# Kernel tuning notes

Measured on AMD Instinct MI355X. Metric: run time of the kernel, lower is better.

The kernel has to match this reference:

```python
import jax, jax.numpy as jnp
import numpy as np

B, P, K_NN, HEADS = 4, 2048, 30, 3
N = B * P


def knn_nbr(feat):
    """Per-cloud exact KNN (no self), returns [N, K_NN+1] global neighbor idx, self appended last.
    Matches torch_geometric knn_graph (loop=False) followed by GATConv add_self_loops=True."""
    f = feat.reshape(B, P, -1)
    sq = jnp.sum(f * f, axis=-1)  # [B,P]
    d = sq[:, :, None] + sq[:, None, :] - 2.0 * jnp.einsum('bpc,bqc->bpq', f, f)
    d = d + jnp.eye(P, dtype=f.dtype)[None] * 1e9  # exclude self
    idx = jax.lax.top_k(-d, K_NN)[1]  # [B,P,K_NN] nearest neighbors
    idx = (idx + (jnp.arange(B) * P)[:, None, None]).reshape(N, K_NN)
    return jnp.concatenate([idx, jnp.arange(N)[:, None]], axis=1)  # self-loop last


def gat(xf, nbr, W, a_src, a_dst, bias):
    """PyG GATConv (v1, concat=True, negative_slope=0.2). nbr: [N,K] incoming sources per node."""
    H, F = a_src.shape
    xh = (xf @ W).reshape(N, H, F)
    s = jnp.sum(xh * a_src, axis=-1)  # [N,H] source scores
    t = jnp.sum(xh * a_dst, axis=-1)  # [N,H] target scores
    e = jax.nn.leaky_relu(s[nbr] + t[:, None, :], 0.2)  # [N,K,H]
    alpha = jax.nn.softmax(e, axis=1)  # edge-softmax over incoming edges
    out = jnp.einsum('nkh,nkhf->nhf', alpha, xh[nbr])
    return out.reshape(N, H * F) + bias


def setup_inputs() -> dict:
    key = jax.random.key(0)
    ks = jax.random.split(key, 48)
    w = lambda k, shape: (jax.random.normal(k, shape, jnp.float32) * 0.1)
    H = HEADS
    inp = {
        'x': jax.random.normal(ks[0], (N, 3), jnp.float32),
        'pos': jax.random.normal(ks[1], (N, 3), jnp.float32),
        'batch': (jnp.arange(N) // P).astype(jnp.int32),
        'w1': w(ks[2], (6, 64 * H)), 'as1': w(ks[3], (H, 64)), 'ad1': w(ks[4], (H, 64)), 'b1': w(ks[5], (64 * H,)),
        'ml1w': w(ks[6], (64 * H, 64)), 'ml1b': w(ks[7], (64,)),
        'w2': w(ks[8], (70, 64 * H)), 'as2': w(ks[9], (H, 64)), 'ad2': w(ks[10], (H, 64)), 'b2': w(ks[11], (64 * H,)),
        'ml2w': w(ks[12], (64 * H, 64)), 'ml2b': w(ks[13], (64,)),
        'w3': w(ks[14], (134, 64 * H)), 'as3': w(ks[15], (H, 64)), 'ad3': w(ks[16], (H, 64)), 'b3': w(ks[17], (64 * H,)),
        'ml3w': w(ks[18], (64 * H, 64)), 'ml3b': w(ks[19], (64,)),
        'w4': w(ks[20], (198, 128 * H)), 'as4': w(ks[21], (H, 128)), 'ad4': w(ks[22], (H, 128)), 'b4': w(ks[23], (128 * H,)),
        'ml4w': w(ks[24], (128 * H, 128)), 'ml4b': w(ks[25], (128,)),
        # fe_mlp: 326 -> 1024 -> 1024 (plain last)
        'few1': w(ks[26], (326, 1024)), 'feb1': w(ks[27], (1024,)),
        'few2': w(ks[28], (1024, 1024)), 'feb2': w(ks[29], (1024,)),
        # head mlp: 1350 -> 256 -> 256 -> 128 -> 50
        'mw1': w(ks[30], (1350, 256)), 'mb1': w(ks[31], (256,)),
        'mw2': w(ks[32], (256, 256)), 'mb2': w(ks[33], (256,)),
        'mw3': w(ks[34], (256, 128)), 'mb3': w(ks[35], (128,)),
        'mw4': w(ks[36], (128, 50)), 'mb4': w(ks[37], (50,)),
    }
    return inp


def reference(x, pos, batch,
              w1, as1, ad1, b1, ml1w, ml1b,
              w2, as2, ad2, b2, ml2w, ml2b,
              w3, as3, ad3, b3, ml3w, ml3b,
              w4, as4, ad4, b4, ml4w, ml4b,
              few1, feb1, few2, feb2,
              mw1, mb1, mw2, mb2, mw3, mb3, mw4, mb4):
    x0 = jnp.concatenate([x, pos], axis=-1)  # [N,6]
    nbr = knn_nbr(x0)
    x1 = gat(x0, nbr, w1, as1, ad1, b1) @ ml1w + ml1b  # [N,64]
    nbr = knn_nbr(x1)
    x2 = gat(jnp.concatenate([x0, x1], 1), nbr, w2, as2, ad2, b2) @ ml2w + ml2b
    nbr = knn_nbr(x2)
    x3 = gat(jnp.concatenate([x0, x1, x2], 1), nbr, w3, as3, ad3, b3) @ ml3w + ml3b
    nbr = knn_nbr(x2)  # faithful to source: 4th graph also built from x2
    x4 = gat(jnp.concatenate([x0, x1, x2, x3], 1), nbr, w4, as4, ad4, b4) @ ml4w + ml4b
    link4 = jnp.concatenate([x0, x1, x2, x3, x4], axis=-1)  # [N,326]
    h = jax.nn.relu(link4 @ few1 + feb1) @ few2 + feb2  # [N,1024]
    g = jnp.max(h, axis=0, keepdims=True)  # global feature (dropout=eval identity)
    lg = jnp.concatenate([link4, jnp.broadcast_to(g, (N, h.shape[1]))], axis=1)
    h = jax.nn.relu(lg @ mw1 + mb1)
    h = jax.nn.relu(h @ mw2 + mb2)
    h = jax.nn.relu(h @ mw3 + mb3)
    out = h @ mw4 + mb4
    return jax.nn.log_softmax(out, axis=1)
```

## Files before the change

### kernel.cpp

```cpp
#include <hip/hip_runtime.h>
#include <hip/hip_bf16.h>
#include <hip/amd_detail/amd_hip_vector_types.h>

#define NPTS 8192
#define PP 2048
#define KNN 30
#define KTOT 31
#define HEADS 3
#define LDH 352
#define NSEG 10

typedef __attribute__((ext_vector_type(8))) short short8;
typedef __attribute__((ext_vector_type(4))) float floatx4;
typedef __attribute__((ext_vector_type(4))) unsigned int uint4_t;
typedef unsigned short ushort_t;
typedef unsigned int uint_t;

__device__ inline ushort_t f2bs(float v) {
    __hip_bfloat16 b = __float2bfloat16(v);
    return *reinterpret_cast<ushort_t*>(&b);
}
__device__ inline float bs2f(ushort_t u) {
    __hip_bfloat16 b = *reinterpret_cast<__hip_bfloat16*>(&u);
    return __bfloat162float(b);
}
__device__ inline void split2(float v, ushort_t& h, ushort_t& l) {
    h = f2bs(v);
    l = f2bs(v - bs2f(h));
}
__device__ inline uint_t fenc(float f) {
    uint_t b = __float_as_uint(f);
    return (b & 0x80000000u) ? ~b : (b | 0x80000000u);
}
__device__ inline float fdec(uint_t e) {
    return __uint_as_float((e & 0x80000000u) ? (e & 0x7FFFFFFFu) : ~e);
}

__global__ void k_build_x0(const float* __restrict__ x, const float* __restrict__ pos,
                           ushort_t* __restrict__ lh, ushort_t* __restrict__ ll) {
    int i = blockIdx.x * blockDim.x + threadIdx.x;
    if (i >= NPTS * 6) return;
    int n = i / 6, c = i % 6;
    float v = (c < 3) ? x[n * 3 + c] : pos[n * 3 + (c - 3)];
    ushort_t h, l; split2(v, h, l);
    lh[(size_t)n * LDH + c] = h;
    ll[(size_t)n * LDH + c] = l;
}

__global__ void k_tw1(const float* __restrict__ x, const float* __restrict__ pos,
                      const float* __restrict__ w1, float* __restrict__ xh) {
    int t = blockIdx.x * blockDim.x + threadIdx.x;
    if (t >= NPTS * 192) return;
    int n = t / 192, j = t % 192;
    float acc = 0.f;
#pragma unroll
    for (int c = 0; c < 3; c++) {
        acc += x[n * 3 + c] * w1[c * 192 + j];
        acc += pos[n * 3 + c] * w1[(3 + c) * 192 + j];
    }
    xh[(size_t)n * 192 + j] = acc;
}

struct WArgs {
    const float* src[NSEG];
    ushort_t* dst[NSEG];
    int K[NSEG], N[NSEG], Kp[NSEG], t0[NSEG];
};
__global__ void k_wsplit_all(WArgs a) {
    int bt = blockIdx.x;
    int si = 0;
#pragma unroll
    for (int i = 1; i < NSEG; i++) if (bt >= a.t0[i]) si = i;
    int t = bt - a.t0[si];
    int K_ = a.K[si], N_ = a.N[si], Kp = a.Kp[si];
    const float* src = a.src[si];
    ushort_t* dh = a.dst[si];
    ushort_t* dl = dh + (size_t)Kp * N_;
    int tX = (N_ + 31) >> 5;
    int k0 = (t / tX) * 32, n0 = (t % tX) * 32;
    __shared__ float tt[32][33];
    int c = threadIdx.x & 31, r8 = threadIdx.x >> 5;
#pragma unroll
    for (int i = 0; i < 4; i++) {
        int r = r8 + i * 8;
        int k = k0 + r, n = n0 + c;
        tt[r][c] = (k < K_ && n < N_) ? src[(size_t)k * N_ + n] : 0.f;
    }
    __syncthreads();
#pragma unroll
    for (int i = 0; i < 4; i++) {
        int r = r8 + i * 8;
        int n = n0 + r, k = k0 + c;
        if (n < N_) {
            float v = tt[c][r];
            ushort_t h, l; split2(v, h, l);
            dh[(size_t)n * Kp + k] = h;
            dl[(size_t)n * Kp + k] = l;
        }
    }
}

template<int MT, int NT>
__global__ __launch_bounds__(256)
void k_mgemm1(const ushort_t* __restrict__ A, int lda,
              const ushort_t* __restrict__ W, int ldw,
              float* __restrict__ Cf, int ldc,
              ushort_t* __restrict__ Ch, int ldh,
              int Ndim, int K,
              const float* __restrict__ bias1, const float* __restrict__ bias2,
              int relu, int lsm, uint_t* __restrict__ gmax,
              const float* __restrict__ asrc, const float* __restrict__ adst,
              float* __restrict__ sb, float* __restrict__ tb, int Fsc, int satomic) {
    constexpr int MTW = MT / 64;
    constexpr int NTT = NT / 16;
    __shared__ ushort_t As[2][MT * 40];
    __shared__ ushort_t Bs[2][NT * 40];
    __shared__ uint_t smax[NT];
    int tid = threadIdx.x;
    int w = tid >> 6, lane = tid & 63;
    int quad = lane >> 4, l16 = lane & 15;
    int m0 = blockIdx.x * MT, n0 = blockIdx.y * NT;
    uint4_t pa[MT / 64], pb[NT / 64];
    auto prefetch = [&](int k0) {
#pragma unroll
        for (int rep = 0; rep < MT / 64; rep++) {
            int idx = tid + rep * 256;
            int row = idx >> 2, q = idx & 3;
            pa[rep] = *(const uint4_t*)(A + (size_t)(m0 + row) * lda + k0 + q * 8);
        }
#pragma unroll
        for (int rep = 0; rep < NT / 64; rep++) {
            int idx = tid + rep * 256;
            int row = idx >> 2, q = idx & 3;
            uint4_t v = {0, 0, 0, 0};
            if (n0 + row < Ndim) v = *(const uint4_t*)(W + (size_t)(n0 + row) * ldw + k0 + q * 8);
            pb[rep] = v;
        }
    };
    auto stage = [&](int buf) {
#pragma unroll
        for (int rep = 0; rep < MT / 64; rep++) {
            int idx = tid + rep * 256;
            int row = idx >> 2, q = idx & 3;
            *(uint4_t*)&As[buf][row * 40 + q * 8] = pa[rep];
        }
#pragma unroll
        for (int rep = 0; rep < NT / 64; rep++) {
            int idx = tid + rep * 256;
            int row = idx >> 2, q = idx & 3;
            *(uint4_t*)&Bs[buf][row * 40 + q * 8] = pb[rep];
        }
    };
    if (gmax) {
        for (int idx = tid; idx < NT; idx += 256) smax[idx] = 0u;
    }
    floatx4 acc[MTW][NTT] = {};
    prefetch(0);
    stage(0);
    __syncthreads();
    int cur = 0;
    for (int k0 = 0; k0 < K; k0 += 32) {
        bool more = (k0 + 32 < K);
        if (more) prefetch(k0 + 32);
        short8 ah[MTW];
#pragma unroll
        for (int mt = 0; mt < MTW; mt++) {
            int r = w * (MT / 4) + mt * 16 + l16;
            ah[mt] = *(short8*)&As[cur][r * 40 + quad * 8];
        }
#pragma unroll
        for (int nt = 0; nt < NTT; nt++) {
            int r = nt * 16 + l16;
            short8 bh = *(short8*)&Bs[cur][r * 40 + quad * 8];
#pragma unroll
            for (int mt = 0; mt < MTW; mt++)
                acc[mt][nt] = __builtin_amdgcn_mfma_f32_16x16x32_bf16(ah[mt], bh, acc[mt][nt], 0, 0, 0);
        }
        if (more) stage(cur ^ 1);
        __syncthreads();
        cur ^= 1;
    }
    if (lsm) {
#pragma unroll
        for (int mt = 0; mt < MTW; mt++) {
#pragma unroll
            for (int r = 0; r < 4; r++) {
                float vv[NTT];
                float mrow = -3e38f;
#pragma unroll
                for (int nt = 0; nt < NTT; nt++) {
                    int n = n0 + nt * 16 + l16;
                    float val = (n < Ndim) ? acc[mt][nt][r] + bias1[n] : -3e38f;
                    vv[nt] = val;
                    mrow = fmaxf(mrow, val);
                }
#pragma unroll
                for (int off = 8; off >= 1; off >>= 1)
                    mrow = fmaxf(mrow, __shfl_xor(mrow, off, 64));
                float s = 0.f;
#pragma unroll
                for (int nt = 0; nt < NTT; nt++)
                    if (vv[nt] > -1e38f) s += expf(vv[nt] - mrow);
#pragma unroll
                for (int off = 8; off >= 1; off >>= 1)
                    s += __shfl_xor(s, off, 64);
                float lse = mrow + logf(s);
                int m = m0 + w * (MT / 4) + mt * 16 + quad * 4 + r;
#pragma unroll
                for (int nt = 0; nt < NTT; nt++) {
                    int n = n0 + nt * 16 + l16;
                    if (n < Ndim) Cf[(size_t)m * ldc + n] = vv[nt] - lse;
                }
            }
        }
        return;
    }
    if (gmax) {
#pragma unroll
        for (int mt = 0; mt < MTW; mt++) {
#pragma unroll
            for (int nt = 0; nt < NTT; nt++) {
#pragma unroll
                for (int r = 0; r < 4; r++) {
                    float v = acc[mt][nt][r] + bias1[nt * 16 + l16 + n0];
                    atomicMax(&smax[nt * 16 + l16], fenc(v));
                }
            }
        }
        __syncthreads();
        for (int idx = tid; idx < NT; idx += 256)
            atomicMax(&gmax[n0 + idx], smax[idx]);
        return;
    }
    if (asrc) {
        int h = n0 / Fsc;
#pragma unroll
        for (int mt = 0; mt < MTW; mt++) {
#pragma unroll
            for (int r = 0; r < 4; r++) {
                float sp = 0.f, tp = 0.f;
#pragma unroll
                for (int nt = 0; nt < NTT; nt++) {
                    float v = acc[mt][nt][r];
                    sp += v * asrc[n0 + nt * 16 + l16];
                    tp += v * adst[n0 + nt * 16 + l16];
                }
#pragma unroll
                for (int off = 8; off >= 1; off >>= 1) {
                    sp += __shfl_xor(sp, off, 64);
                    tp += __shfl_xor(tp, off, 64);
                }
                if (l16 == 0) {
                    int m = m0 + w * (MT / 4) + mt * 16 + quad * 4 + r;
                    if (satomic) {
                        atomicAdd(&sb[m * HEADS + h], sp);
                        atomicAdd(&tb[m * HEADS + h], tp);
                    } else {
                        sb[m * HEADS + h] = sp;
                        tb[m * HEADS + h] = tp;
                    }
                }
            }
        }
    }
#pragma unroll
    for (int mt = 0; mt < MTW; mt++) {
#pragma unroll
        for (int nt = 0; nt < NTT; nt++) {
#pragma unroll
            for (int r = 0; r < 4; r++) {
                int m = m0 + w * (MT / 4) + mt * 16 + quad * 4 + r;
                int n = n0 + nt * 16 + l16;
                if (n < Ndim) {
                    float v = acc[mt][nt][r];
                    if (bias1) v += bias1[n];
                    if (bias2) v += bias2[n];
                    if (relu && v < 0.f) v = 0.f;
                    if (Cf) Cf[(size_t)m * ldc + n] = v;
                    if (Ch) Ch[(size_t)m * ldh + n] = f2bs(v);
                }
            }
        }
    }
}

__global__ __launch_bounds__(256)
void k_mgemm3(const ushort_t* __restrict__ Ah, const ushort_t* __restrict__ Al, int lda,
              const ushort_t* __restrict__ Wh, const ushort_t* __restrict__ Wl, int ldw,
              float* __restrict__ Cf, int ldc,
              int Ndim, int K,
              const float* __restrict__ asrc, const float* __restrict__ adst,
              float* __restrict__ sb, float* __restrict__ tb, int Fsc) {
    constexpr int NTT = 4;
    __shared__ ushort_t AsH[64 * 40], BsH[64 * 40], AsL[64 * 40], BsL[64 * 40];
    int tid = threadIdx.x;
    int w = tid >> 6, lane = tid & 63;
    int quad = lane >> 4, l16 = lane & 15;
    int m0 = blockIdx.y * 64, n0 = blockIdx.x * 64;
    floatx4 acc[NTT] = {};
    for (int k0 = 0; k0 < K; k0 += 32) {
        {
            int row = tid >> 2, q = tid & 3;
            size_t go = (size_t)(m0 + row) * lda + k0 + q * 8;
            *(uint4_t*)&AsH[row * 40 + q * 8] = *(const uint4_t*)(Ah + go);
            *(uint4_t*)&AsL[row * 40 + q * 8] = *(const uint4_t*)(Al + go);
            uint4_t vh = {0, 0, 0, 0}, vl = {0, 0, 0, 0};
            size_t gw = (size_t)(n0 + row) * ldw + k0 + q * 8;
            if (n0 + row < Ndim) { vh = *(const uint4_t*)(Wh + gw); vl = *(const uint4_t*)(Wl + gw); }
            *(uint4_t*)&BsH[row * 40 + q * 8] = vh;
            *(uint4_t*)&BsL[row * 40 + q * 8] = vl;
        }
        __syncthreads();
        short8 ah, al;
        {
            int r = w * 16 + l16;
            ah = *(short8*)&AsH[r * 40 + quad * 8];
            al = *(short8*)&AsL[r * 40 + quad * 8];
        }
#pragma unroll
        for (int nt = 0; nt < NTT; nt++) {
            int r = nt * 16 + l16;
            short8 bh = *(short8*)&BsH[r * 40 + quad * 8];
            short8 bl = *(short8*)&BsL[r * 40 + quad * 8];
            acc[nt] = __builtin_amdgcn_mfma_f32_16x16x32_bf16(ah, bh, acc[nt], 0, 0, 0);
            acc[nt] = __builtin_amdgcn_mfma_f32_16x16x32_bf16(ah, bl, acc[nt], 0, 0, 0);
            acc[nt] = __builtin_amdgcn_mfma_f32_16x16x32_bf16(al, bh, acc[nt], 0, 0, 0);
        }
        __syncthreads();
    }
    if (asrc) {
        int h = n0 / Fsc;
#pragma unroll
        for (int r = 0; r < 4; r++) {
            float sp = 0.f, tp = 0.f;
#pragma unroll
            for (int nt = 0; nt < NTT; nt++) {
                float v = acc[nt][r];
                sp += v * asrc[n0 + nt * 16 + l16];
                tp += v * adst[n0 + nt * 16 + l16];
            }
#pragma unroll
            for (int off = 8; off >= 1; off >>= 1) {
                sp += __shfl_xor(sp, off, 64);
                tp += __shfl_xor(tp, off, 64);
            }
            if (l16 == 0) {
                int m = m0 + w * 16 + quad * 4 + r;
                sb[m * HEADS + h] = sp;
                tb[m * HEADS + h] = tp;
            }
        }
    }
#pragma unroll
    for (int nt = 0; nt < NTT; nt++) {
#pragma unroll
        for (int r = 0; r < 4; r++) {
            int m = m0 + w * 16 + quad * 4 + r;
            int n = n0 + nt * 16 + l16;
            if (n < Ndim) Cf[(size_t)m * ldc + n] = acc[nt][r];
        }
    }
}

template<int N_, int NPB>
__global__ __launch_bounds__(NPB * N_)
void k_vgemm(const float* __restrict__ A, int lda, int K_,
             const float* __restrict__ W, const float* __restrict__ bias,
             ushort_t* __restrict__ Ch, ushort_t* __restrict__ Cl, int ldh,
             float* __restrict__ Cf, int ldc, int relu) {
    constexpr int KT = 64;
    __shared__ float Ws[KT * N_];
    __shared__ float As[NPB * KT];
    int t = threadIdx.x;
    int n0 = blockIdx.x * NPB;
    int node = t / N_, j = t % N_;
    float acc = bias ? bias[j] : 0.f;
    for (int k0 = 0; k0 < K_; k0 += KT) {
        for (int idx = t; idx < KT * N_; idx += NPB * N_)
            Ws[idx] = W[(size_t)(k0 + idx / N_) * N_ + idx % N_];
        for (int idx = t; idx < NPB * KT; idx += NPB * N_)
            As[idx] = A[(size_t)(n0 + idx / KT) * lda + k0 + idx % KT];
        __syncthreads();
#pragma unroll
        for (int kk = 0; kk < KT; kk++)
            acc += As[node * KT + kk] * Ws[kk * N_ + j];
        __syncthreads();
    }
    if (relu && acc < 0.f) acc = 0.f;
    size_t m = n0 + node;
    if (Cf) Cf[m * ldc + j] = acc;
    if (Ch) {
        ushort_t h = f2bs(acc);
        Ch[m * ldh + j] = h;
        if (Cl) Cl[m * ldh + j] = f2bs(acc - bs2f(h));
    }
}

__global__ __launch_bounds__(256)
void k_mdist(const ushort_t* __restrict__ Lh, const ushort_t* __restrict__ Ll,
             int co, int C, uint_t* __restrict__ keys) {
    __shared__ ushort_t AsH[128 * 40], AsL[128 * 40], BsH[64 * 40], BsL[64 * 40];
    __shared__ float sqa[128], sqb[64];
    int tid = threadIdx.x;
    int w = tid >> 6, lane = tid & 63;
    int quad = lane >> 4, l16 = lane & 15;
    int b = blockIdx.z, cb = b * PP;
    int i0 = blockIdx.y * 128, j0 = blockIdx.x * 64;
    floatx4 acc[2][4] = {};
    float sacc = 0.f;
    for (int k0 = 0; k0 < C; k0 += 32) {
#pragma unroll
        for (int rep = 0; rep < 8; rep++) {
            int d = tid + rep * 256;
            int row = d >> 4, c2 = d & 15;
            size_t gi = ((size_t)(cb + i0 + row) * LDH + co + k0 + c2 * 2) >> 1;
            *(uint_t*)&AsH[row * 40 + c2 * 2] = ((const uint_t*)Lh)[gi];
            *(uint_t*)&AsL[row * 40 + c2 * 2] = ((const uint_t*)Ll)[gi];
        }
#pragma unroll
        for (int rep = 0; rep < 4; rep++) {
            int d = tid + rep * 256;
            int row = d >> 4, c2 = d & 15;
            size_t gi = ((size_t)(cb + j0 + row) * LDH + co + k0 + c2 * 2) >> 1;
            *(uint_t*)&BsH[row * 40 + c2 * 2] = ((const uint_t*)Lh)[gi];
            *(uint_t*)&BsL[row * 40 + c2 * 2] = ((const uint_t*)Ll)[gi];
        }
        __syncthreads();
        if (tid < 128) {
#pragma unroll
            for (int kk = 0; kk < 16; kk++) {
                uint_t ph = *(uint_t*)&AsH[tid * 40 + kk * 2];
                uint_t pl = *(uint_t*)&AsL[tid * 40 + kk * 2];
                float v0 = bs2f((ushort_t)(ph & 0xFFFFu)) + bs2f((ushort_t)(pl & 0xFFFFu));
                sacc += v0 * v0;
                float v1 = bs2f((ushort_t)(ph >> 16)) + bs2f((ushort_t)(pl >> 16));
                sacc += v1 * v1;
            }
        } else if (tid < 192) {
            int row = tid - 128;
#pragma unroll
            for (int kk = 0; kk < 16; kk++) {
                uint_t ph = *(uint_t*)&BsH[row * 40 + kk * 2];
                uint_t pl = *(uint_t*)&BsL[row * 40 + kk * 2];
                float v0 = bs2f((ushort_t)(ph & 0xFFFFu)) + bs2f((ushort_t)(pl & 0xFFFFu));
                sacc += v0 * v0;
                float v1 = bs2f((ushort_t)(ph >> 16)) + bs2f((ushort_t)(pl >> 16));
                sacc += v1 * v1;
            }
        }
        short8 ah[2], al[2];
#pragma unroll
        for (int mt = 0; mt < 2; mt++) {
            int r = w * 32 + mt * 16 + l16;
            ah[mt] = *(short8*)&AsH[r * 40 + quad * 8];
            al[mt] = *(short8*)&AsL[r * 40 + quad * 8];
        }
#pragma unroll
        for (int nt = 0; nt < 4; nt++) {
            int r = nt * 16 + l16;
            short8 bh = *(short8*)&BsH[r * 40 + quad * 8];
            short8 bl = *(short8*)&BsL[r * 40 + quad * 8];
#pragma unroll
            for (int mt = 0; mt < 2; mt++) {
                acc[mt][nt] = __builtin_amdgcn_mfma_f32_16x16x32_bf16(ah[mt], bh, acc[mt][nt], 0, 0, 0);
                acc[mt][nt] = __builtin_amdgcn_mfma_f32_16x16x32_bf16(ah[mt], bl, acc[mt][nt], 0, 0, 0);
                acc[mt][nt] = __builtin_amdgcn_mfma_f32_16x16x32_bf16(al[mt], bh, acc[mt][nt], 0, 0, 0);
            }
        }
        __syncthreads();
    }
    if (tid < 128) sqa[tid] = sacc;
    else if (tid < 192) sqb[tid - 128] = sacc;
    __syncthreads();
#pragma unroll
    for (int mt = 0; mt < 2; mt++) {
#pragma unroll
        for (int nt = 0; nt < 4; nt++) {
#pragma unroll
            for (int r = 0; r < 4; r++) {
                int li = w * 32 + mt * 16 + quad * 4 + r;
                int lj = nt * 16 + l16;
                int il = i0 + li, jl = j0 + lj;
                float dd = sqa[li] + sqb[lj] - 2.f * acc[mt][nt][r];
                dd = (il == jl) ? 3e9f : fmaxf(dd, 0.f);
                uint_t key = (__float_as_uint(dd) & 0xFFFFF800u) | (uint_t)jl;
                __builtin_nontemporal_store(key, &keys[(size_t)(cb + il) * PP + jl]);
            }
        }
    }
}

__global__ __launch_bounds__(256)
void k_topk(const uint_t* __restrict__ keys, int* __restrict__ nbr) {
    int r = blockIdx.x * 4 + (threadIdx.x >> 6);
    int lane = threadIdx.x & 63;
    int base = (r / PP) * PP;
    const uint_t* row = keys + (size_t)r * PP;
    uint_t v[32];
#pragma unroll
    for (int j = 0; j < 8; j++)
        *(uint4_t*)&v[j * 4] = *(const uint4_t*)(row + lane * 4 + j * 256);
    uint_t g[8];
#pragma unroll
    for (int j = 0; j < 8; j++)
        g[j] = min(min(v[j * 4], v[j * 4 + 1]), min(v[j * 4 + 2], v[j * 4 + 3]));
    uint_t lv = g[0];
#pragma unroll
    for (int j = 1; j < 8; j++) lv = min(lv, g[j]);
    for (int sel = 0; sel < KNN; sel++) {
        uint_t bk = lv;
#pragma unroll
        for (int off = 32; off > 0; off >>= 1)
            bk = min(bk, (uint_t)__shfl_xor((int)bk, off, 64));
        uint_t bks = __builtin_amdgcn_readfirstlane(bk);
        if (lane == 0) nbr[r * KTOT + sel] = base + (int)(bks & 0x7FFu);
        int grp = (int)((bks & 0x7FFu) >> 8);
#pragma unroll
        for (int jj = 0; jj < 8; jj++)
            if (grp == jj) {
#pragma unroll
                for (int t = 0; t < 4; t++)
                    v[jj * 4 + t] = (v[jj * 4 + t] == bks) ? 0xFFFFFFFFu : v[jj * 4 + t];
                g[jj] = min(min(v[jj * 4], v[jj * 4 + 1]), min(v[jj * 4 + 2], v[jj * 4 + 3]));
            }
        lv = g[0];
#pragma unroll
        for (int j = 1; j < 8; j++) lv = min(lv, g[j]);
    }
    if (lane == 0) nbr[r * KTOT + KNN] = r;
}

__global__ void k_scores(const float* __restrict__ xh, int F,
                         const float* __restrict__ a_src,
                         const float* __restrict__ a_dst,
                         float* __restrict__ s, float* __restrict__ t) {
    int g = blockIdx.x * blockDim.x + threadIdx.x;
    if (g >= NPTS * HEADS) return;
    int n = g / HEADS, h = g % HEADS;
    const float* xr = xh + (size_t)n * (HEADS * F) + h * F;
    float ss = 0.f, tt = 0.f;
    for (int f = 0; f < F; f++) {
        float v = xr[f];
        ss += v * a_src[h * F + f];
        tt += v * a_dst[h * F + f];
    }
    s[g] = ss;
    t[g] = tt;
}

__global__ void k_gat(const float* __restrict__ xh, int F,
                      const float* __restrict__ s, const float* __restrict__ t,
                      const int* __restrict__ nbr,
                      const float* __restrict__ bias,
                      float* __restrict__ outf, ushort_t* __restrict__ oh) {
    int HF = HEADS * F;
    __shared__ int srcs[KTOT];
    __shared__ float alpha[KTOT * HEADS];
    int i = (blockIdx.x & 3) * PP + (blockIdx.x >> 2);
    int tid = threadIdx.x;
    if (tid < KTOT) srcs[tid] = nbr[i * KTOT + tid];
    __syncthreads();
    if (tid < KTOT * HEADS) {
        int k = tid / HEADS, h = tid % HEADS;
        float e = s[srcs[k] * HEADS + h] + t[i * HEADS + h];
        if (e < 0.f) e *= 0.2f;
        alpha[tid] = e;
    }
    __syncthreads();
    if (tid < HEADS) {
        int h = tid;
        float m = -3e38f;
        for (int k = 0; k < KTOT; k++) m = fmaxf(m, alpha[k * HEADS + h]);
        float sum = 0.f;
        for (int k = 0; k < KTOT; k++) {
            float ex = expf(alpha[k * HEADS + h] - m);
            alpha[k * HEADS + h] = ex;
            sum += ex;
        }
        float inv = 1.f / sum;
        for (int k = 0; k < KTOT; k++) alpha[k * HEADS + h] *= inv;
    }
    __syncthreads();
    int h = tid / F;
    float acc = 0.f;
    for (int k = 0; k < KTOT; k++)
        acc += alpha[k * HEADS + h] * xh[(size_t)srcs[k] * HF + tid];
    float v = acc + bias[tid];
    if (oh) oh[(size_t)i * HF + tid] = f2bs(v);
    else outf[(size_t)i * HF + tid] = v;
}

__global__ void k_gproj(const uint_t* __restrict__ genc,
                        const float* __restrict__ mw1,
                        const float* __restrict__ mb1,
                        float* __restrict__ gproj) {
    __shared__ float gs[128];
    int kb = blockIdx.x;
    int t = threadIdx.x;
    if (t < 128) gs[t] = fdec(genc[kb * 128 + t]);
    __syncthreads();
    float acc = (kb == 0) ? mb1[t] : 0.f;
    for (int k = 0; k < 128; k++)
        acc += gs[k] * mw1[(size_t)(326 + kb * 128 + k) * 256 + t];
    atomicAdd(&gproj[t], acc);
}

struct WT { ushort_t *h, *l; int kp; };

extern "C" void kernel_launch(void* const* d_in, const int* in_sizes, int n_in,
                              void* d_out, int out_size, void* d_ws, size_t ws_size,
                              hipStream_t stream) {
    (void)in_sizes; (void)n_in; (void)out_size; (void)ws_size;
    const float* x    = (const float*)d_in[0];
    const float* pos  = (const float*)d_in[1];
    const float* w1   = (const float*)d_in[3];
    const float* as1  = (const float*)d_in[4];
    const float* ad1  = (const float*)d_in[5];
    const float* b1   = (const float*)d_in[6];
    const float* ml1w = (const float*)d_in[7];
    const float* ml1b = (const float*)d_in[8];
    const float* w2   = (const float*)d_in[9];
    const float* as2  = (const float*)d_in[10];
    const float* ad2  = (const float*)d_in[11];
    const float* b2   = (const float*)d_in[12];
    const float* ml2w = (const float*)d_in[13];
    const float* ml2b = (const float*)d_in[14];
    const float* w3   = (const float*)d_in[15];
    const float* as3  = (const float*)d_in[16];
    const float* ad3  = (const float*)d_in[17];
    const float* b3   = (const float*)d_in[18];
    const float* ml3w = (const float*)d_in[19];
    const float* ml3b = (const float*)d_in[20];
    const float* w4   = (const float*)d_in[21];
    const float* as4  = (const float*)d_in[22];
    const float* ad4  = (const float*)d_in[23];
    const float* b4   = (const float*)d_in[24];
    const float* ml4w = (const float*)d_in[25];
    const float* ml4b = (const float*)d_in[26];
    const float* few1 = (const float*)d_in[27];
    const float* feb1 = (const float*)d_in[28];
    const float* few2 = (const float*)d_in[29];
    const float* feb2 = (const float*)d_in[30];
    const float* mw1  = (const float*)d_in[31];
    const float* mb1  = (const float*)d_in[32];
    const float* mw2  = (const float*)d_in[33];
    const float* mb2  = (const float*)d_in[34];
    const float* mw3  = (const float*)d_in[35];
    const float* mb3  = (const float*)d_in[36];
    const float* mw4  = (const float*)d_in[37];
    const float* mb4  = (const float*)d_in[38];

    float* Wb = (float*)d_ws;
    size_t off = 0;
    auto alloc = [&](size_t n) { float* p = Wb + off; off += (n + 63) & ~(size_t)63; return p; };

    float*    dist = alloc((size_t)NPTS * PP);
    ushort_t* l4h  = (ushort_t*)alloc((size_t)NPTS * LDH / 2);
    ushort_t* l4l  = (ushort_t*)alloc((size_t)NPTS * LDH / 2);
    float*    gof  = alloc((size_t)NPTS * 384);
    ushort_t* goh  = (ushort_t*)alloc((size_t)NPTS * 384 / 2);
    float* sbuf  = alloc((size_t)NPTS * HEADS);
    float* tbuf  = alloc((size_t)NPTS * HEADS);
    float* s4   = alloc((size_t)NPTS * HEADS);
    float* t4   = alloc((size_t)NPTS * HEADS);
    uint_t* genc = (uint_t*)alloc(1024);
    float* gproj = alloc(256);
    int*   nbr   = (int*)alloc((size_t)NPTS * KTOT);
    ushort_t* wtpool = (ushort_t*)alloc(1831168 + 128);

    char* d0 = (char*)dist;
    uint_t*   dkey = (uint_t*)dist;
    float*    xh   = dist;
    ushort_t* hah  = (ushort_t*)d0;
    ushort_t* bBh  = (ushort_t*)(d0 + (size_t)NPTS * 1024 * 2);
    ushort_t* bAh = (ushort_t*)gof;
    ushort_t* bCh = (ushort_t*)gof;

    hipMemsetAsync(l4h, 0, (size_t)NPTS * LDH * 4, stream);
    hipMemsetAsync(gproj, 0, 256 * 4, stream);
    hipMemsetAsync(genc, 0, 1024 * 4, stream);
    hipMemsetAsync(s4, 0, (size_t)NPTS * HEADS * 2 * 4, stream);

    WArgs wa;
    WT wt[NSEG];
    {
        const float* srcs[NSEG] = {w2, w3, w4, ml4w, few1, few2, mw1, mw2, mw3, mw4};
        int Ks[NSEG] = {70, 134, 198, 384, 326, 1024, 326, 256, 256, 128};
        int Ns[NSEG] = {192, 192, 384, 128, 1024, 1024, 256, 256, 128, 50};
        size_t wo = 0; int tiles = 0;
        for (int i = 0; i < NSEG; i++) {
            int kp = (Ks[i] + 31) & ~31;
            wa.src[i] = srcs[i];
            wa.dst[i] = wtpool + wo;
            wa.K[i] = Ks[i]; wa.N[i] = Ns[i]; wa.Kp[i] = kp;
            wa.t0[i] = tiles;
            wt[i] = { wtpool + wo, wtpool + wo + (size_t)kp * Ns[i], kp };
            wo += (size_t)2 * kp * Ns[i];
            tiles += (kp / 32) * ((Ns[i] + 31) / 32);
        }
        k_wsplit_all<<<tiles, 256, 0, stream>>>(wa);
    }
    WT tw2 = wt[0], tw3 = wt[1], tw4 = wt[2], tml4 = wt[3], tfe1 = wt[4], tfe2 = wt[5],
       tmw1 = wt[6], tmw2 = wt[7], tmw3 = wt[8], tmw4 = wt[9];

    auto mg3 = [&](const ushort_t* Ah, const ushort_t* Al, int lda, WT t,
                   float* Cf, int ldc, int Nd, int K,
                   const float* asrc, const float* adst, float* sb, float* tb, int Fsc) {
        dim3 g((Nd + 63) / 64, NPTS / 64);
        k_mgemm3<<<g, 256, 0, stream>>>(Ah, Al, lda, t.h, t.l, t.kp, Cf, ldc, Nd, K,
                                        asrc, adst, sb, tb, Fsc);
    };
    auto mg1 = [&](int MT, int NT, const ushort_t* Ah, int lda, WT t,
                   float* Cf, int ldc, ushort_t* Ch, int ldhh,
                   int Nd, int K, const float* bb1, const float* bb2,
                   int relu, int lsm, uint_t* gmax,
                   const float* asrc, const float* adst, float* sb, float* tb,
                   int Fsc, int satomic) {
        dim3 g(NPTS / MT, (Nd + NT - 1) / NT);
        if (MT == 128 && NT == 64)
            k_mgemm1<128, 64><<<g, 256, 0, stream>>>(Ah, lda, t.h, t.kp, Cf, ldc, Ch, ldhh, Nd, K,
                bb1, bb2, relu, lsm, gmax, asrc, adst, sb, tb, Fsc, satomic);
        else
            k_mgemm1<64, 64><<<g, 256, 0, stream>>>(Ah, lda, t.h, t.kp, Cf, ldc, Ch, ldhh, Nd, K,
                bb1, bb2, relu, lsm, gmax, asrc, adst, sb, tb, Fsc, satomic);
    };

    dim3 dgrid(PP / 64, PP / 128, 4);
    k_build_x0<<<(NPTS * 6 + 255) / 256, 256, 0, stream>>>(x, pos, l4h, l4l);

    k_mdist<<<dgrid, 256, 0, stream>>>(l4h, l4l, 0, 6, dkey);
    k_topk<<<NPTS / 4, 256, 0, stream>>>(dkey, nbr);
    k_tw1<<<(NPTS * 192 + 255) / 256, 256, 0, stream>>>(x, pos, w1, xh);
    k_scores<<<(NPTS * HEADS + 255) / 256, 256, 0, stream>>>(xh, 64, as1, ad1, sbuf, tbuf);
    k_gat<<<NPTS, 192, 0, stream>>>(xh, 64, sbuf, tbuf, nbr, b1, gof, nullptr);
    k_vgemm<64, 4><<<NPTS / 4, 256, 0, stream>>>(gof, 192, 192, ml1w, ml1b,
        l4h + 6, l4l + 6, LDH, nullptr, 0, 0);

    k_mdist<<<dgrid, 256, 0, stream>>>(l4h, l4l, 6, 64, dkey);
    k_topk<<<NPTS / 4, 256, 0, stream>>>(dkey, nbr);
    mg3(l4h, l4l, LDH, tw2, xh, 192, 192, 70, as2, ad2, sbuf, tbuf, 64);
    k_gat<<<NPTS, 192, 0, stream>>>(xh, 64, sbuf, tbuf, nbr, b2, gof, nullptr);
    k_vgemm<64, 4><<<NPTS / 4, 256, 0, stream>>>(gof, 192, 192, ml2w, ml2b,
        l4h + 70, l4l + 70, LDH, nullptr, 0, 0);

    k_mdist<<<dgrid, 256, 0, stream>>>(l4h, l4l, 70, 64, dkey);
    k_topk<<<NPTS / 4, 256, 0, stream>>>(dkey, nbr);
    mg1(64, 64, l4h, LDH, tw3, xh, 192, nullptr, 0, 192, 134, nullptr, nullptr, 0, 0, nullptr,
        as3, ad3, sbuf, tbuf, 64, 0);
    k_gat<<<NPTS, 192, 0, stream>>>(xh, 64, sbuf, tbuf, nbr, b3, gof, nullptr);
    k_vgemm<64, 4><<<NPTS / 4, 256, 0, stream>>>(gof, 192, 192, ml3w, ml3b,
        l4h + 134, nullptr, LDH, nullptr, 0, 0);

    mg1(64, 64, l4h, LDH, tw4, xh, 384, nullptr, 0, 384, 198, nullptr, nullptr, 0, 0, nullptr,
        as4, ad4, s4, t4, 128, 1);
    k_gat<<<NPTS, 384, 0, stream>>>(xh, 128, s4, t4, nbr, b4, nullptr, goh);
    mg1(64, 64, goh, 384, tml4, nullptr, 0, l4h + 198, LDH, 128, 384, ml4b, nullptr, 0, 0, nullptr,
        nullptr, nullptr, nullptr, nullptr, 1, 0);

    mg1(128, 64, l4h, LDH, tfe1, nullptr, 0, hah, 1024, 1024, 326, feb1, nullptr, 1, 0, nullptr,
        nullptr, nullptr, nullptr, nullptr, 1, 0);
    mg1(128, 64, hah, 1024, tfe2, nullptr, 0, nullptr, 0, 1024, 1024, feb2, nullptr, 0, 0, genc,
        nullptr, nullptr, nullptr, nullptr, 1, 0);
    k_gproj<<<8, 256, 0, stream>>>(genc, mw1, mb1, gproj);

    mg1(128, 64, l4h, LDH, tmw1, nullptr, 0, bAh, 256, 256, 326, nullptr, gproj, 1, 0, nullptr,
        nullptr, nullptr, nullptr, nullptr, 1, 0);
    mg1(128, 64, bAh, 256, tmw2, nullptr, 0, bBh, 256, 256, 256, mb2, nullptr, 1, 0, nullptr,
        nullptr, nullptr, nullptr, nullptr, 1, 0);
    mg1(64, 64, bBh, 256, tmw3, nullptr, 0, bCh, 128, 128, 256, mb3, nullptr, 1, 0, nullptr,
        nullptr, nullptr, nullptr, nullptr, 1, 0);
    mg1(64, 64, bCh, 128, tmw4, (float*)d_out, 50, nullptr, 0, 50, 128, mb4, nullptr, 0, 1, nullptr,
        nullptr, nullptr, nullptr, nullptr, 1, 0);
}
```

Baseline: 615.3 us.

## Fold GAT output projection and attention vectors into combined weights

Precomputes combined weights W·mlW per head, plus W·a_src and W·a_dst columns and a folded bias, in a new k_combine kernel. Each GAT layer's per-node GEMM then directly produces projected per-head features and attention scores. The aggregation kernel sums the per-head contributions and writes bf16 hi/lo into the feature buffer, which removes the separate score kernel, the post-GAT linear GEMMs and the intermediate buffers. It also switches the fe1/fe2 GEMMs to 128x128 tiles. The risk is changed rounding from reassociating the linear maps, which could slightly alter the KNN neighbour selection in later layers.

```diff
diff --git a/kernel.cpp b/kernel.cpp
--- a/kernel.cpp
+++ b/kernel.cpp
@@ -8,7 +8,9 @@
 #define KTOT 31
 #define HEADS 3
 #define LDH 352
-#define NSEG 10
+#define NSEG 9
+#define LDZ 200
+#define LDZ4 392
 
 typedef __attribute__((ext_vector_type(8))) short short8;
 typedef __attribute__((ext_vector_type(4))) float floatx4;
@@ -47,18 +49,61 @@
     ll[(size_t)n * LDH + c] = l;
 }
 
+struct CArgs {
+    const float *w[4], *mlw[4], *as_[4], *ad[4], *b[4], *mlb[4];
+    float *wc[4], *bc[4];
+    int K[4], F[4], t0[4];
+};
+__global__ void k_combine(CArgs a) {
+    int bt = blockIdx.x, si = 0;
+#pragma unroll
+    for (int i = 1; i < 4; i++) if (bt >= a.t0[i]) si = i;
+    int t = (bt - a.t0[si]) * 256 + threadIdx.x;
+    int K_ = a.K[si], F_ = a.F[si];
+    int NC = 3 * F_ + 6;
+    const float* w = a.w[si];
+    const float* mlw = a.mlw[si];
+    if (t < K_ * NC) {
+        int k = t / NC, c = t % NC;
+        float acc = 0.f;
+        if (c < 3 * F_) {
+            int h = c / F_, j = c % F_;
+            for (int f = 0; f < F_; f++)
+                acc += w[(size_t)k * 3 * F_ + h * F_ + f] * mlw[(size_t)(h * F_ + f) * F_ + j];
+        } else if (c < 3 * F_ + 3) {
+            int h = c - 3 * F_;
+            const float* av = a.as_[si];
+            for (int f = 0; f < F_; f++)
+                acc += w[(size_t)k * 3 * F_ + h * F_ + f] * av[h * F_ + f];
+        } else {
+            int h = c - 3 * F_ - 3;
+            const float* av = a.ad[si];
+            for (int f = 0; f < F_; f++)
+                acc += w[(size_t)k * 3 * F_ + h * F_ + f] * av[h * F_ + f];
+        }
+        a.wc[si][t] = acc;
+    } else if (t < K_ * NC + F_) {
+        int j = t - K_ * NC;
+        float acc = a.mlb[si][j];
+        const float* b = a.b[si];
+        for (int c = 0; c < 3 * F_; c++)
+            acc += b[c] * mlw[(size_t)c * F_ + j];
+        a.bc[si][j] = acc;
+    }
+}
+
 __global__ void k_tw1(const float* __restrict__ x, const float* __restrict__ pos,
-                      const float* __restrict__ w1, float* __restrict__ xh) {
+                      const float* __restrict__ wc, float* __restrict__ z) {
     int t = blockIdx.x * blockDim.x + threadIdx.x;
-    if (t >= NPTS * 192) return;
-    int n = t / 192, j = t % 192;
+    if (t >= NPTS * 198) return;
+    int n = t / 198, j = t % 198;
     float acc = 0.f;
 #pragma unroll
     for (int c = 0; c < 3; c++) {
-        acc += x[n * 3 + c] * w1[c * 192 + j];
-        acc += pos[n * 3 + c] * w1[(3 + c) * 192 + j];
-    }
-    xh[(size_t)n * 192 + j] = acc;
+        acc += x[n * 3 + c] * wc[c * 198 + j];
+        acc += pos[n * 3 + c] * wc[(3 + c) * 198 + j];
+    }
+    z[(size_t)n * LDZ + j] = acc;
 }
 
 struct WArgs {
@@ -108,9 +153,7 @@
               ushort_t* __restrict__ Ch, int ldh,
               int Ndim, int K,
               const float* __restrict__ bias1, const float* __restrict__ bias2,
-              int relu, int lsm, uint_t* __restrict__ gmax,
-              const float* __restrict__ asrc, const float* __restrict__ adst,
-              float* __restrict__ sb, float* __restrict__ tb, int Fsc, int satomic) {
+              int relu, int lsm, uint_t* __restrict__ gmax) {
     constexpr int MTW = MT / 64;
     constexpr int NTT = NT / 16;
     __shared__ ushort_t As[2][MT * 40];
@@ -231,37 +274,6 @@
         for (int idx = tid; idx < NT; idx += 256)
             atomicMax(&gmax[n0 + idx], smax[idx]);
         return;
-    }
-    if (asrc) {
-        int h = n0 / Fsc;
-#pragma unroll
-        for (int mt = 0; mt < MTW; mt++) {
-#pragma unroll
-            for (int r = 0; r < 4; r++) {
-                float sp = 0.f, tp = 0.f;
-#pragma unroll
-                for (int nt = 0; nt < NTT; nt++) {
-                    float v = acc[mt][nt][r];
-                    sp += v * asrc[n0 + nt * 16 + l16];
-                    tp += v * adst[n0 + nt * 16 + l16];
-                }
-#pragma unroll
-                for (int off = 8; off >= 1; off >>= 1) {
-                    sp += __shfl_xor(sp, off, 64);
-                    tp += __shfl_xor(tp, off, 64);
-                }
-                if (l16 == 0) {
-                    int m = m0 + w * (MT / 4) + mt * 16 + quad * 4 + r;
-                    if (satomic) {
-                        atomicAdd(&sb[m * HEADS + h], sp);
-                        atomicAdd(&tb[m * HEADS + h], tp);
-                    } else {
-                        sb[m * HEADS + h] = sp;
-                        tb[m * HEADS + h] = tp;
-                    }
-                }
-            }
-        }
     }
 #pragma unroll
     for (int mt = 0; mt < MTW; mt++) {
@@ -288,9 +300,7 @@
 void k_mgemm3(const ushort_t* __restrict__ Ah, const ushort_t* __restrict__ Al, int lda,
               const ushort_t* __restrict__ Wh, const ushort_t* __restrict__ Wl, int ldw,
               float* __restrict__ Cf, int ldc,
-              int Ndim, int K,
-              const float* __restrict__ asrc, const float* __restrict__ adst,
-              float* __restrict__ sb, float* __restrict__ tb, int Fsc) {
+              int Ndim, int K) {
     constexpr int NTT = 4;
     __shared__ ushort_t AsH[64 * 40], BsH[64 * 40], AsL[64 * 40], BsL[64 * 40];
     int tid = threadIdx.x;
@@ -328,29 +338,6 @@
         }
         __syncthreads();
     }
-    if (asrc) {
-        int h = n0 / Fsc;
-#pragma unroll
-        for (int r = 0; r < 4; r++) {
-            float sp = 0.f, tp = 0.f;
-#pragma unroll
-            for (int nt = 0; nt < NTT; nt++) {
-                float v = acc[nt][r];
-                sp += v * asrc[n0 + nt * 16 + l16];
-                tp += v * adst[n0 + nt * 16 + l16];
-            }
-#pragma unroll
-            for (int off = 8; off >= 1; off >>= 1) {
-                sp += __shfl_xor(sp, off, 64);
-                tp += __shfl_xor(tp, off, 64);
-            }
-            if (l16 == 0) {
-                int m = m0 + w * 16 + quad * 4 + r;
-                sb[m * HEADS + h] = sp;
-                tb[m * HEADS + h] = tp;
-            }
-        }
-    }
 #pragma unroll
     for (int nt = 0; nt < NTT; nt++) {
 #pragma unroll
@@ -359,40 +346,6 @@
             int n = n0 + nt * 16 + l16;
             if (n < Ndim) Cf[(size_t)m * ldc + n] = acc[nt][r];
         }
-    }
-}
-
-template<int N_, int NPB>
-__global__ __launch_bounds__(NPB * N_)
-void k_vgemm(const float* __restrict__ A, int lda, int K_,
-             const float* __restrict__ W, const float* __restrict__ bias,
-             ushort_t* __restrict__ Ch, ushort_t* __restrict__ Cl, int ldh,
-             float* __restrict__ Cf, int ldc, int relu) {
-    constexpr int KT = 64;
-    __shared__ float Ws[KT * N_];
-    __shared__ float As[NPB * KT];
-    int t = threadIdx.x;
-    int n0 = blockIdx.x * NPB;
-    int node = t / N_, j = t % N_;
-    float acc = bias ? bias[j] : 0.f;
-    for (int k0 = 0; k0 < K_; k0 += KT) {
-        for (int idx = t; idx < KT * N_; idx += NPB * N_)
-            Ws[idx] = W[(size_t)(k0 + idx / N_) * N_ + idx % N_];
-        for (int idx = t; idx < NPB * KT; idx += NPB * N_)
-            As[idx] = A[(size_t)(n0 + idx / KT) * lda + k0 + idx % KT];
-        __syncthreads();
-#pragma unroll
-        for (int kk = 0; kk < KT; kk++)
-            acc += As[node * KT + kk] * Ws[kk * N_ + j];
-        __syncthreads();
-    }
-    if (relu && acc < 0.f) acc = 0.f;
-    size_t m = n0 + node;
-    if (Cf) Cf[m * ldc + j] = acc;
-    if (Ch) {
-        ushort_t h = f2bs(acc);
-        Ch[m * ldh + j] = h;
-        if (Cl) Cl[m * ldh + j] = f2bs(acc - bs2f(h));
     }
 }
 
@@ -530,39 +483,22 @@
     if (lane == 0) nbr[r * KTOT + KNN] = r;
 }
 
-__global__ void k_scores(const float* __restrict__ xh, int F,
-                         const float* __restrict__ a_src,
-                         const float* __restrict__ a_dst,
-                         float* __restrict__ s, float* __restrict__ t) {
-    int g = blockIdx.x * blockDim.x + threadIdx.x;
-    if (g >= NPTS * HEADS) return;
-    int n = g / HEADS, h = g % HEADS;
-    const float* xr = xh + (size_t)n * (HEADS * F) + h * F;
-    float ss = 0.f, tt = 0.f;
-    for (int f = 0; f < F; f++) {
-        float v = xr[f];
-        ss += v * a_src[h * F + f];
-        tt += v * a_dst[h * F + f];
-    }
-    s[g] = ss;
-    t[g] = tt;
-}
-
-__global__ void k_gat(const float* __restrict__ xh, int F,
-                      const float* __restrict__ s, const float* __restrict__ t,
-                      const int* __restrict__ nbr,
-                      const float* __restrict__ bias,
-                      float* __restrict__ outf, ushort_t* __restrict__ oh) {
-    int HF = HEADS * F;
+template<int F>
+__global__ __launch_bounds__(3 * F)
+void k_gat2(const float* __restrict__ z, int ldz,
+            const int* __restrict__ nbr,
+            const float* __restrict__ bc,
+            ushort_t* __restrict__ dh, ushort_t* __restrict__ dl) {
     __shared__ int srcs[KTOT];
     __shared__ float alpha[KTOT * HEADS];
+    __shared__ float part[HEADS * F];
     int i = (blockIdx.x & 3) * PP + (blockIdx.x >> 2);
     int tid = threadIdx.x;
     if (tid < KTOT) srcs[tid] = nbr[i * KTOT + tid];
     __syncthreads();
     if (tid < KTOT * HEADS) {
         int k = tid / HEADS, h = tid % HEADS;
-        float e = s[srcs[k] * HEADS + h] + t[i * HEADS + h];
+        float e = z[(size_t)srcs[k] * ldz + 3 * F + h] + z[(size_t)i * ldz + 3 * F + 3 + h];
         if (e < 0.f) e *= 0.2f;
         alpha[tid] = e;
     }
@@ -581,13 +517,18 @@
         for (int k = 0; k < KTOT; k++) alpha[k * HEADS + h] *= inv;
     }
     __syncthreads();
-    int h = tid / F;
+    int h = tid / F, j = tid % F;
     float acc = 0.f;
     for (int k = 0; k < KTOT; k++)
-        acc += alpha[k * HEADS + h] * xh[(size_t)srcs[k] * HF + tid];
-    float v = acc + bias[tid];
-    if (oh) oh[(size_t)i * HF + tid] = f2bs(v);
-    else outf[(size_t)i * HF + tid] = v;
+        acc += alpha[k * HEADS + h] * z[(size_t)srcs[k] * ldz + h * F + j];
+    part[h * F + j] = acc;
+    __syncthreads();
+    if (tid < F) {
+        float v = part[tid] + part[F + tid] + part[2 * F + tid] + bc[tid];
+        ushort_t hi = f2bs(v);
+        dh[(size_t)i * LDH + tid] = hi;
+        if (dl) dl[(size_t)i * LDH + tid] = f2bs(v - bs2f(hi));
+    }
 }
 
 __global__ void k_gproj(const uint_t* __restrict__ genc,
@@ -657,36 +598,58 @@
     float*    dist = alloc((size_t)NPTS * PP);
     ushort_t* l4h  = (ushort_t*)alloc((size_t)NPTS * LDH / 2);
     ushort_t* l4l  = (ushort_t*)alloc((size_t)NPTS * LDH / 2);
-    float*    gof  = alloc((size_t)NPTS * 384);
-    ushort_t* goh  = (ushort_t*)alloc((size_t)NPTS * 384 / 2);
-    float* sbuf  = alloc((size_t)NPTS * HEADS);
-    float* tbuf  = alloc((size_t)NPTS * HEADS);
-    float* s4   = alloc((size_t)NPTS * HEADS);
-    float* t4   = alloc((size_t)NPTS * HEADS);
     uint_t* genc = (uint_t*)alloc(1024);
     float* gproj = alloc(256);
     int*   nbr   = (int*)alloc((size_t)NPTS * KTOT);
-    ushort_t* wtpool = (ushort_t*)alloc(1831168 + 128);
+    ushort_t* wtpool = (ushort_t*)alloc(1742336);
+    float* wc1 = alloc(6 * 198);
+    float* wc2 = alloc(70 * 198);
+    float* wc3 = alloc(134 * 198);
+    float* wc4 = alloc(198 * 390);
+    float* bc1 = alloc(64);
+    float* bc2 = alloc(64);
+    float* bc3 = alloc(64);
+    float* bc4 = alloc(128);
 
     char* d0 = (char*)dist;
     uint_t*   dkey = (uint_t*)dist;
-    float*    xh   = dist;
+    float*    z    = dist;
     ushort_t* hah  = (ushort_t*)d0;
     ushort_t* bBh  = (ushort_t*)(d0 + (size_t)NPTS * 1024 * 2);
-    ushort_t* bAh = (ushort_t*)gof;
-    ushort_t* bCh = (ushort_t*)gof;
+    ushort_t* bAh = (ushort_t*)d0;
+    ushort_t* bCh = (ushort_t*)d0;
 
     hipMemsetAsync(l4h, 0, (size_t)NPTS * LDH * 4, stream);
     hipMemsetAsync(gproj, 0, 256 * 4, stream);
     hipMemsetAsync(genc, 0, 1024 * 4, stream);
-    hipMemsetAsync(s4, 0, (size_t)NPTS * HEADS * 2 * 4, stream);
+
+    {
+        CArgs ca;
+        const float* ws_[4] = {w1, w2, w3, w4};
+        const float* mlws[4] = {ml1w, ml2w, ml3w, ml4w};
+        const float* ass[4] = {as1, as2, as3, as4};
+        const float* ads[4] = {ad1, ad2, ad3, ad4};
+        const float* bs_[4] = {b1, b2, b3, b4};
+        const float* mlbs[4] = {ml1b, ml2b, ml3b, ml4b};
+        float* wcs[4] = {wc1, wc2, wc3, wc4};
+        float* bcs[4] = {bc1, bc2, bc3, bc4};
+        int Ks[4] = {6, 70, 134, 198}, Fs[4] = {64, 64, 64, 128};
+        int t = 0;
+        for (int i = 0; i < 4; i++) {
+            ca.w[i] = ws_[i]; ca.mlw[i] = mlws[i]; ca.as_[i] = ass[i]; ca.ad[i] = ads[i];
+            ca.b[i] = bs_[i]; ca.mlb[i] = mlbs[i]; ca.wc[i] = wcs[i]; ca.bc[i] = bcs[i];
+            ca.K[i] = Ks[i]; ca.F[i] = Fs[i]; ca.t0[i] = t;
+            t += (Ks[i] * (3 * Fs[i] + 6) + Fs[i] + 255) / 256;
+        }
+        k_combine<<<t, 256, 0, stream>>>(ca);
+    }
 
     WArgs wa;
     WT wt[NSEG];
     {
-        const float* srcs[NSEG] = {w2, w3, w4, ml4w, few1, few2, mw1, mw2, mw3, mw4};
-        int Ks[NSEG] = {70, 134, 198, 384, 326, 1024, 326, 256, 256, 128};
-        int Ns[NSEG] = {192, 192, 384, 128, 1024, 1024, 256, 256, 128, 50};
+        const float* srcs[NSEG] = {wc2, wc3, wc4, few1, few2, mw1, mw2, mw3, mw4};
+        int Ks[NSEG] = {70, 134, 198, 326, 1024, 326, 256, 256, 128};
+        int Ns[NSEG] = {198, 198, 390, 1024, 1024, 256, 256, 128, 50};
         size_t wo = 0; int tiles = 0;
         for (int i = 0; i < NSEG; i++) {
             int kp = (Ks[i] + 31) & ~31;
@@ -700,29 +663,28 @@
         }
         k_wsplit_all<<<tiles, 256, 0, stream>>>(wa);
     }
-    WT tw2 = wt[0], tw3 = wt[1], tw4 = wt[2], tml4 = wt[3], tfe1 = wt[4], tfe2 = wt[5],
-       tmw1 = wt[6], tmw2 = wt[7], tmw3 = wt[8], tmw4 = wt[9];
+    WT tw2 = wt[0], tw3 = wt[1], tw4 = wt[2], tfe1 = wt[3], tfe2 = wt[4],
+       tmw1 = wt[5], tmw2 = wt[6], tmw3 = wt[7], tmw4 = wt[8];
 
     auto mg3 = [&](const ushort_t* Ah, const ushort_t* Al, int lda, WT t,
-                   float* Cf, int ldc, int Nd, int K,
-                   const float* asrc, const float* adst, float* sb, float* tb, int Fsc) {
+                   float* Cf, int ldc, int Nd, int K) {
         dim3 g((Nd + 63) / 64, NPTS / 64);
-        k_mgemm3<<<g, 256, 0, stream>>>(Ah, Al, lda, t.h, t.l, t.kp, Cf, ldc, Nd, K,
-                                        asrc, adst, sb, tb, Fsc);
+        k_mgemm3<<<g, 256, 0, stream>>>(Ah, Al, lda, t.h, t.l, t.kp, Cf, ldc, Nd, K);
     };
     auto mg1 = [&](int MT, int NT, const ushort_t* Ah, int lda, WT t,
                    float* Cf, int ldc, ushort_t* Ch, int ldhh,
                    int Nd, int K, const float* bb1, const float* bb2,
-                   int relu, int lsm, uint_t* gmax,
-                   const float* asrc, const float* adst, float* sb, float* tb,
-                   int Fsc, int satomic) {
+                   int relu, int lsm, uint_t* gmax) {
         dim3 g(NPTS / MT, (Nd + NT - 1) / NT);
-        if (MT == 128 && NT == 64)
+        if (MT == 128 && NT == 128)
+            k_mgemm1<128, 128><<<g, 256, 0, stream>>>(Ah, lda, t.h, t.kp, Cf, ldc, Ch, ldhh, Nd, K,
+                bb1, bb2, relu, lsm, gmax);
+        else if (MT == 128)
             k_mgemm1<128, 64><<<g, 256, 0, stream>>>(Ah, lda, t.h, t.kp, Cf, ldc, Ch, ldhh, Nd, K,
-                bb1, bb2, relu, lsm, gmax, asrc, adst, sb, tb, Fsc, satomic);
+                bb1, bb2, relu, lsm, gmax);
         else
             k_mgemm1<64, 64><<<g, 256, 0, stream>>>(Ah, lda, t.h, t.kp, Cf, ldc, Ch, ldhh, Nd, K,
-                bb1, bb2, relu, lsm, gmax, asrc, adst, sb, tb, Fsc, satomic);
+                bb1, bb2, relu, lsm, gmax);
     };
 
     dim3 dgrid(PP / 64, PP / 128, 4);
@@ -730,45 +692,28 @@
 
     k_mdist<<<dgrid, 256, 0, stream>>>(l4h, l4l, 0, 6, dkey);
     k_topk<<<NPTS / 4, 256, 0, stream>>>(dkey, nbr);
-    k_tw1<<<(NPTS * 192 + 255) / 256, 256, 0, stream>>>(x, pos, w1, xh);
-    k_scores<<<(NPTS * HEADS + 255) / 256, 256, 0, stream>>>(xh, 64, as1, ad1, sbuf, tbuf);
-    k_gat<<<NPTS, 192, 0, stream>>>(xh, 64, sbuf, tbuf, nbr, b1, gof, nullptr);
-    k_vgemm<64, 4><<<NPTS / 4, 256, 0, stream>>>(gof, 192, 192, ml1w, ml1b,
-        l4h + 6, l4l + 6, LDH, nullptr, 0, 0);
+    k_tw1<<<(NPTS * 198 + 255) / 256, 256, 0, stream>>>(x, pos, wc1, z);
+    k_gat2<64><<<NPTS, 192, 0, stream>>>(z, LDZ, nbr, bc1, l4h + 6, l4l + 6);
 
     k_mdist<<<dgrid, 256, 0, stream>>>(l4h, l4l, 6, 64, dkey);
     k_topk<<<NPTS / 4, 256, 0, stream>>>(dkey, nbr);
-    mg3(l4h, l4l, LDH, tw2, xh, 192, 192, 70, as2, ad2, sbuf, tbuf, 64);
-    k_gat<<<NPTS, 192, 0, stream>>>(xh, 64, sbuf, tbuf, nbr, b2, gof, nullptr);
-    k_vgemm<64, 4><<<NPTS / 4, 256, 0, stream>>>(gof, 192, 192, ml2w, ml2b,
-        l4h + 70, l4l + 70, LDH, nullptr, 0, 0);
+    mg3(l4h, l4l, LDH, tw2, z, LDZ, 198, 70);
+    k_gat2<64><<<NPTS, 192, 0, stream>>>(z, LDZ, nbr, bc2, l4h + 70, l4l + 70);
 
     k_mdist<<<dgrid, 256, 0, stream>>>(l4h, l4l, 70, 64, dkey);
     k_topk<<<NPTS / 4, 256, 0, stream>>>(dkey, nbr);
-    mg1(64, 64, l4h, LDH, tw3, xh, 192, nullptr, 0, 192, 134, nullptr, nullptr, 0, 0, nullptr,
-        as3, ad3, sbuf, tbuf, 64, 0);
-    k_gat<<<NPTS, 192, 0, stream>>>(xh, 64, sbuf, tbuf, nbr, b3, gof, nullptr);
-    k_vgemm<64, 4><<<NPTS / 4, 256, 0, stream>>>(gof, 192, 192, ml3w, ml3b,
-        l4h + 134, nullptr, LDH, nullptr, 0, 0);
-
-    mg1(64, 64, l4h, LDH, tw4, xh, 384, nullptr, 0, 384, 198, nullptr, nullptr, 0, 0, nullptr,
-        as4, ad4, s4, t4, 128, 1);
-    k_gat<<<NPTS, 384, 0, stream>>>(xh, 128, s4, t4, nbr, b4, nullptr, goh);
-    mg1(64, 64, goh, 384, tml4, nullptr, 0, l4h + 198, LDH, 128, 384, ml4b, nullptr, 0, 0, nullptr,
-        nullptr, nullptr, nullptr, nullptr, 1, 0);
-
-    mg1(128, 64, l4h, LDH, tfe1, nullptr, 0, hah, 1024, 1024, 326, feb1, nullptr, 1, 0, nullptr,
-        nullptr, nullptr, nullptr, nullptr, 1, 0);
-    mg1(128, 64, hah, 1024, tfe2, nullptr, 0, nullptr, 0, 1024, 1024, feb2, nullptr, 0, 0, genc,
-        nullptr, nullptr, nullptr, nullptr, 1, 0);
+    mg1(64, 64, l4h, LDH, tw3, z, LDZ, nullptr, 0, 198, 134, nullptr, nullptr, 0, 0, nullptr);
+    k_gat2<64><<<NPTS, 192, 0, stream>>>(z, LDZ, nbr, bc3, l4h + 134, nullptr);
+
+    mg1(64, 64, l4h, LDH, tw4, z, LDZ4, nullptr, 0, 390, 198, nullptr, nullptr, 0, 0, nullptr);
+    k_gat2<128><<<NPTS, 384, 0, stream>>>(z, LDZ4, nbr, bc4, l4h + 198, nullptr);
+
+    mg1(128, 128, l4h, LDH, tfe1, nullptr, 0, hah, 1024, 1024, 326, feb1, nullptr, 1, 0, nullptr);
+    mg1(128, 128, hah, 1024, tfe2, nullptr, 0, nullptr, 0, 1024, 1024, feb2, nullptr, 0, 0, genc);
     k_gproj<<<8, 256, 0, stream>>>(genc, mw1, mb1, gproj);
 
-    mg1(128, 64, l4h, LDH, tmw1, nullptr, 0, bAh, 256, 256, 326, nullptr, gproj, 1, 0, nullptr,
-        nullptr, nullptr, nullptr, nullptr, 1, 0);
-    mg1(128, 64, bAh, 256, tmw2, nullptr, 0, bBh, 256, 256, 256, mb2, nullptr, 1, 0, nullptr,
-        nullptr, nullptr, nullptr, nullptr, 1, 0);
-    mg1(64, 64, bBh, 256, tmw3, nullptr, 0, bCh, 128, 128, 256, mb3, nullptr, 1, 0, nullptr,
-        nullptr, nullptr, nullptr, nullptr, 1, 0);
-    mg1(64, 64, bCh, 128, tmw4, (float*)d_out, 50, nullptr, 0, 50, 128, mb4, nullptr, 0, 1, nullptr,
-        nullptr, nullptr, nullptr, nullptr, 1, 0);
-}
+    mg1(128, 64, l4h, LDH, tmw1, nullptr, 0, bAh, 256, 256, 326, nullptr, gproj, 1, 0, nullptr);
+    mg1(128, 64, bAh, 256, tmw2, nullptr, 0, bBh, 256, 256, 256, mb2, nullptr, 1, 0, nullptr);
+    mg1(64, 64, bBh, 256, tmw3, nullptr, 0, bCh, 128, 128, 256, mb3, nullptr, 1, 0, nullptr);
+    mg1(64, 64, bCh, 128, tmw4, (float*)d_out, 50, nullptr, 0, 50, 128, mb4, nullptr, 0, 1, nullptr);
+}
```

Result: slower. 634.4 us (+3.1%).
